# Performance work log

Measured on AMD Instinct MI355X. Metric: run time of the kernel, lower is better.

## Reference

```python
import jax, jax.numpy as jnp
import numpy as np

B, C, H, W = 8, 256, 64, 64
CQK = C // 8  # 32


def setup_inputs() -> dict:
    key = jax.random.key(0)
    ks = jax.random.split(key, 8)
    s = 0.05
    return {
        "x": jax.random.normal(ks[0], (B, C, H, W), dtype=jnp.float32),
        "wq": jax.random.normal(ks[1], (CQK, C), dtype=jnp.float32) * s,
        "bq": jax.random.normal(ks[2], (CQK,), dtype=jnp.float32) * s,
        "wk": jax.random.normal(ks[3], (CQK, C), dtype=jnp.float32) * s,
        "bk": jax.random.normal(ks[4], (CQK,), dtype=jnp.float32) * s,
        "wv": jax.random.normal(ks[5], (C, C), dtype=jnp.float32) * s,
        "bv": jax.random.normal(ks[6], (C,), dtype=jnp.float32) * s,
        "gamma": jax.random.normal(ks[7], (1,), dtype=jnp.float32),
    }


def reference(x, wq, bq, wk, bk, wv, bv, gamma):
    b, c, h, w = x.shape
    xf = x.reshape(b, c, h * w)  # [B, C, N]
    # conv1d kernel-size-1 == per-token linear over channels
    f = jnp.einsum('oc,bcn->bon', wq, xf) + bq[None, :, None]  # [B, C/8, N]
    g = jnp.einsum('oc,bcn->bon', wk, xf) + bk[None, :, None]  # [B, C/8, N]
    hh = jnp.einsum('oc,bcn->bon', wv, xf) + bv[None, :, None]  # [B, C, N]
    # scores[b, i, j] = sum_o f[b, o, i] * g[b, o, j]; NO 1/sqrt(d) scaling
    scores = jnp.einsum('boi,boj->bij', f, g)  # [B, N, N]
    # softmax over dim=1 (the f/query index axis), as in the original
    beta = jax.nn.softmax(scores, axis=1)
    # o[b, c, j] = gamma * sum_i hh[b, c, i] * beta[b, i, j] + xf
    o = gamma[0] * jnp.einsum('bci,bij->bcj', hh, beta) + xf
    return o.reshape(b, c, h, w)
```

## Files before the change

### kernel.cpp

```cpp
#include <hip/hip_runtime.h>
#include <stdint.h>

#define B_ 8
#define C_ 256
#define N_ 4096
#define LOG2E 1.44269504088896f
#define NSHIFT_L2E (-14.0f * 1.44269504088896f)

typedef _Float16 half8 __attribute__((ext_vector_type(8)));
typedef _Float16 half4 __attribute__((ext_vector_type(4)));
typedef __fp16  fp16x2 __attribute__((ext_vector_type(2)));
typedef float floatx4 __attribute__((ext_vector_type(4)));

__global__ __launch_bounds__(256) void k_wprep(const float* __restrict__ wq, const float* __restrict__ bq,
                                               const float* __restrict__ wk, const float* __restrict__ bk,
                                               const float* __restrict__ wv, const float* __restrict__ bv,
                                               _Float16* __restrict__ Whf, float* __restrict__ Bh) {
    int r = blockIdx.x;
    int t = threadIdx.x;
    const float* src;
    float bias;
    if (r < 32)      { src = wq + r * 256;        bias = bq[r]; }
    else if (r < 64) { src = wk + (r - 32) * 256; bias = bk[r - 32]; }
    else             { src = wv + (r - 64) * 256; bias = bv[r - 64]; }
    Whf[(t >> 3) * 2560 + r * 8 + (t & 7)] = (_Float16)src[t];
    if (t == 0) Bh[r] = bias;
}

__global__ __launch_bounds__(256) void k_proj(const float* __restrict__ x,
                                              const _Float16* __restrict__ Whf,
                                              const float* __restrict__ Bh,
                                              _Float16* __restrict__ Kf,
                                              _Float16* __restrict__ Qf,
                                              _Float16* __restrict__ Vf) {
    __shared__ float xtile[64 * 65];
    __shared__ _Float16 As[64 * 264] __attribute__((aligned(16)));
    int id = blockIdx.x;
    int b  = id & 7;
    int i0 = (id >> 3) * 64;
    int t = threadIdx.x;
    int w = t >> 6, lane = t & 63, col = lane & 15, q = lane >> 4;
    const float* xb = x + (size_t)b * C_ * N_ + i0;
    int cr = t >> 4;
    int ip = (t & 15) * 4;
    float4 r0[4], r1[4];
#pragma unroll
    for (int k = 0; k < 4; ++k)
        r0[k] = *(const float4*)&xb[(size_t)(cr + 16 * k) * N_ + ip];
    for (int cc = 0; cc < 4; ++cc) {
        if (cc < 3) {
#pragma unroll
            for (int k = 0; k < 4; ++k)
                r1[k] = *(const float4*)&xb[(size_t)((cc + 1) * 64 + cr + 16 * k) * N_ + ip];
        }
#pragma unroll
        for (int k = 0; k < 4; ++k)
            *(float4*)&xtile[(cr + 16 * k) * 65 + ip] = r0[k];
        __syncthreads();
        int i = t & 63, cb2 = (t >> 6) * 16;
        float v[16];
#pragma unroll
        for (int k = 0; k < 16; ++k) v[k] = xtile[(cb2 + k) * 65 + i];
        half8 h0, h1;
#pragma unroll
        for (int k = 0; k < 8; ++k) { h0[k] = (_Float16)v[k]; h1[k] = (_Float16)v[8 + k]; }
        *(half8*)&As[i * 264 + cc * 64 + cb2] = h0;
        *(half8*)&As[i * 264 + cc * 64 + cb2 + 8] = h1;
        __syncthreads();
#pragma unroll
        for (int k = 0; k < 4; ++k) r0[k] = r1[k];
    }
    floatx4 acc[4][5];
#pragma unroll
    for (int mt = 0; mt < 4; ++mt)
#pragma unroll
        for (int nt = 0; nt < 5; ++nt) acc[mt][nt] = (floatx4){0.f, 0.f, 0.f, 0.f};
#pragma unroll
    for (int kc = 0; kc < 8; ++kc) {
        half8 a[4], bf[5];
#pragma unroll
        for (int nt = 0; nt < 5; ++nt)
            bf[nt] = *(const half8*)&Whf[(kc * 4 + q) * 2560 + (w * 80 + nt * 16 + col) * 8];
#pragma unroll
        for (int mt = 0; mt < 4; ++mt)
            a[mt] = *(const half8*)&As[(mt * 16 + col) * 264 + kc * 32 + q * 8];
#pragma unroll
        for (int mt = 0; mt < 4; ++mt)
#pragma unroll
            for (int nt = 0; nt < 5; ++nt)
                acc[mt][nt] = __builtin_amdgcn_mfma_f32_16x16x32_f16(a[mt], bf[nt], acc[mt][nt], 0, 0, 0);
    }
#pragma unroll
    for (int nt = 0; nt < 5; ++nt) {
        int n = w * 80 + nt * 16 + col;
        float bias = Bh[n];
        if (n < 32) {
#pragma unroll
            for (int mt = 0; mt < 4; ++mt)
#pragma unroll
                for (int r = 0; r < 4; ++r) {
                    int i = i0 + mt * 16 + q * 4 + r;
                    Kf[((((size_t)b * 128 + (i >> 5)) * 4 + (n >> 3)) * 32 + (i & 31)) * 8 + (n & 7)]
                        = (_Float16)((acc[mt][nt][r] + bias) * LOG2E);
                }
        } else if (n < 64) {
            int n2 = n - 32;
#pragma unroll
            for (int mt = 0; mt < 4; ++mt)
#pragma unroll
                for (int r = 0; r < 4; ++r) {
                    int j = i0 + mt * 16 + q * 4 + r;
                    Qf[((((size_t)b * 128 + (j >> 5)) * 4 + (n2 >> 3)) * 32 + (j & 31)) * 8 + (n2 & 7)]
                        = (_Float16)(acc[mt][nt][r] + bias);
                }
        } else {
            int c = n - 64;
#pragma unroll
            for (int mt = 0; mt < 4; ++mt) {
                int ib = (i0 >> 4) + mt;
                half4 v4;
#pragma unroll
                for (int r = 0; r < 4; ++r) v4[r] = (_Float16)(acc[mt][nt][r] + bias);
                *(half4*)&Vf[(((size_t)b * 256 + ib) * 256 + c) * 16 + q * 4] = v4;
            }
        }
    }
}

#define PS_BUF 4096

#define ATTN_STEP(IT, VCUR, VNXT, ROFF, WOFF)                                     \
    {                                                                             \
        if ((IT) < 63) {                                                          \
            _Pragma("unroll")                                                     \
            for (int ct = 0; ct < 2; ++ct) {                                      \
                VNXT[ct * 2 + 0] = *(const half8*)(pV0 + ct * 256);               \
                VNXT[ct * 2 + 1] = *(const half8*)(pV1 + ct * 256);               \
            }                                                                     \
            pV0 += 16384; pV1 += 16384;                                           \
            aKn0 = *(const half8*)(pK);                                           \
            aKn1 = *(const half8*)(pK + 128);                                     \
            pK += 2048;                                                           \
        }                                                                         \
        _Pragma("unroll")                                                         \
        for (int kk = 0; kk < 2; ++kk) {                                          \
            half8 bfr[4];                                                         \
            _Pragma("unroll")                                                     \
            for (int jt = 0; jt < 4; ++jt)                                        \
                bfr[jt] = *(const half8*)&PsF[(ROFF) + jt * 1024 + (kk ? ro1 : ro0)]; \
            _Pragma("unroll")                                                     \
            for (int ct = 0; ct < 2; ++ct)                                        \
                _Pragma("unroll")                                                 \
                for (int jt = 0; jt < 4; ++jt)                                    \
                    acc[ct][jt] = __builtin_amdgcn_mfma_f32_16x16x32_f16(         \
                        VCUR[ct * 2 + kk], bfr[jt], acc[ct][jt], 0, 0, 0);        \
        }                                                                         \
        if ((IT) < 63) {                                                          \
            _Pragma("unroll")                                                     \
            for (int itl = 0; itl < 2; ++itl) {                                   \
                floatx4 s = __builtin_amdgcn_mfma_f32_16x16x32_f16(               \
                    itl ? aKn1 : aKn0, bq, cns, 0, 0, 0);                         \
                float p0 = exp2f(s[0]);                                           \
                float p1 = exp2f(s[1]);                                           \
                float p2 = exp2f(s[2]);                                           \
                float p3 = exp2f(s[3]);                                           \
                lacc += (p0 + p1) + (p2 + p3);                                    \
                union { fp16x2 v; uint32_t u; } plo, phi;                         \
                plo.v = __builtin_amdgcn_cvt_pkrtz(p0, p1);                       \
                phi.v = __builtin_amdgcn_cvt_pkrtz(p2, p3);                       \
                uint2 pw; pw.x = plo.u; pw.y = phi.u;                             \
                *(uint2*)&PsF[(WOFF) + (itl ? wo1 : wo0)] = pw;                   \
            }                                                                     \
        }                                                                         \
        asm volatile("s_waitcnt lgkmcnt(0)\n\ts_barrier" ::: "memory");           \
    }

__global__ __launch_bounds__(512, 4) void k_attn(const _Float16* __restrict__ Kf,
                                                 const _Float16* __restrict__ Qf,
                                                 const _Float16* __restrict__ Vf,
                                                 const float* __restrict__ x,
                                                 const float* __restrict__ gptr,
                                                 float* __restrict__ out) {
    __shared__ _Float16 PsF[2 * PS_BUF] __attribute__((aligned(16)));
    __shared__ float Lp[2][64];
    int id = blockIdx.x;
    int b  = id & 7;
    int j0 = (id >> 3) * 64;
    int t = threadIdx.x;
    int w = t >> 6, lane = t & 63, col = lane & 15, q = lane >> 4;
    int jts = w & 3, ihs = w >> 2;
    int cw  = w * 32;
    const _Float16* Kfb = Kf + (size_t)b * 131072;
    const _Float16* Qfb = Qf + (size_t)b * 131072;
    const _Float16* Vfb = Vf + (size_t)b * 1048576;
    const _Float16* pK  = Kfb + ((ihs * 4 + q) * 32 + col) * 8;
    const _Float16* pV0 = Vfb + ((q >> 1) * 256 + cw + col) * 16 + (q & 1) * 8;
    const _Float16* pV1 = pV0 + 8192;
    const int cswz = col & 7;
    const int ro0 = col * 64 + ((q ^ cswz) << 3);
    const int ro1 = ro0 ^ 32;
    const int wo0 = (jts * 16 + col) * 64 + (((ihs << 2) ^ (q >> 1) ^ cswz) << 3) + (q & 1) * 4;
    const int wo1 = wo0 ^ 16;
    const floatx4 cns = {NSHIFT_L2E, NSHIFT_L2E, NSHIFT_L2E, NSHIFT_L2E};
    floatx4 acc[2][4];
#pragma unroll
    for (int ct = 0; ct < 2; ++ct)
#pragma unroll
        for (int jt = 0; jt < 4; ++jt) acc[ct][jt] = (floatx4){0.f, 0.f, 0.f, 0.f};
    float lacc = 0.f;
    half8 vA[4], vB[4], aKn0, aKn1;
#pragma unroll
    for (int ct = 0; ct < 2; ++ct) {
        vA[ct * 2 + 0] = *(const half8*)(pV0 + ct * 256);
        vA[ct * 2 + 1] = *(const half8*)(pV1 + ct * 256);
    }
    pV0 += 16384; pV1 += 16384;
    aKn0 = *(const half8*)(pK);
    aKn1 = *(const half8*)(pK + 128);
    pK += 2048;
    int jj = j0 + jts * 16;
    half8 bq = *(const half8*)&Qfb[(((jj >> 5) * 4 + q) * 32 + ((jj & 31) + col)) * 8];
#pragma unroll
    for (int itl = 0; itl < 2; ++itl) {
        floatx4 s = __builtin_amdgcn_mfma_f32_16x16x32_f16(itl ? aKn1 : aKn0, bq, cns, 0, 0, 0);
        float p0 = exp2f(s[0]);
        float p1 = exp2f(s[1]);
        float p2 = exp2f(s[2]);
        float p3 = exp2f(s[3]);
        lacc += (p0 + p1) + (p2 + p3);
        union { fp16x2 v; uint32_t u; } plo, phi;
        plo.v = __builtin_amdgcn_cvt_pkrtz(p0, p1);
        phi.v = __builtin_amdgcn_cvt_pkrtz(p2, p3);
        uint2 pw; pw.x = plo.u; pw.y = phi.u;
        *(uint2*)&PsF[itl ? wo1 : wo0] = pw;
    }
    asm volatile("s_waitcnt lgkmcnt(0)\n\ts_barrier" ::: "memory");
    for (int m = 0; m < 32; ++m) {
        int it = m * 2;
        ATTN_STEP(it,     vA, vB, 0,      PS_BUF)
        ATTN_STEP(it + 1, vB, vA, PS_BUF, 0)
    }
    lacc += __shfl_xor(lacc, 16, 64);
    lacc += __shfl_xor(lacc, 32, 64);
    if (lane < 16) Lp[ihs][jts * 16 + lane] = lacc;
    __syncthreads();
    float gamma = gptr[0];
    const float* xb = x + (size_t)b * C_ * N_;
    float* ob = out + (size_t)b * C_ * N_;
#pragma unroll
    for (int jt = 0; jt < 4; ++jt) {
        int jl = jt * 16 + col;
        float li = 1.0f / (Lp[0][jl] + Lp[1][jl]);
        int j = j0 + jl;
#pragma unroll
        for (int ct = 0; ct < 2; ++ct)
#pragma unroll
            for (int r = 0; r < 4; ++r) {
                int c = cw + ct * 16 + q * 4 + r;
                size_t off = (size_t)c * N_ + j;
                ob[off] = gamma * acc[ct][jt][r] * li + xb[off];
            }
    }
}

extern "C" void kernel_launch(void* const* d_in, const int* in_sizes, int n_in,
                              void* d_out, int out_size, void* d_ws, size_t ws_size,
                              hipStream_t stream) {
    const float* x  = (const float*)d_in[0];
    const float* wq = (const float*)d_in[1];
    const float* bq = (const float*)d_in[2];
    const float* wk = (const float*)d_in[3];
    const float* bk = (const float*)d_in[4];
    const float* wv = (const float*)d_in[5];
    const float* bv = (const float*)d_in[6];
    const float* gm = (const float*)d_in[7];
    float* out = (float*)d_out;
    char* ws = (char*)d_ws;
    _Float16* Vf  = (_Float16*)ws;
    _Float16* Kf  = (_Float16*)(ws + 16777216);
    _Float16* Qf  = (_Float16*)(ws + 18874368);
    _Float16* Whf = (_Float16*)(ws + 20971520);
    float*    Bh  = (float*)(ws + 21135360);

    k_wprep<<<dim3(320), 256, 0, stream>>>(wq, bq, wk, bk, wv, bv, Whf, Bh);
    k_proj<<<dim3(512), 256, 0, stream>>>(x, Whf, Bh, Kf, Qf, Vf);
    k_proj<<<dim3(512), 256, 0, stream>>>(x, Whf, Bh, Kf, Qf, Vf);
    k_attn<<<dim3(512), 512, 0, stream>>>(Kf, Qf, Vf, x, gm, out);
}
```

Measured before the change: 229.8 us.

## Fuse weight conversion into projection kernel, drop duplicate launch, stage K/Q in LDS

Removes the separate weight-prep kernel: the projection kernel now reads fp32 weights and biases directly and converts them to fp16 in registers. It also drops the duplicated k_proj launch, which recomputed the same outputs. K and Q results are staged in shared memory (reusing the x-tile buffer) and written out with coalesced 16-byte stores instead of scattered 2-byte stores. The cost is redundant weight reads and conversions in every block, though the weights are small and likely cached.

```diff
diff --git a/kernel.cpp b/kernel.cpp
--- a/kernel.cpp
+++ b/kernel.cpp
@@ -12,29 +12,17 @@
 typedef __fp16  fp16x2 __attribute__((ext_vector_type(2)));
 typedef float floatx4 __attribute__((ext_vector_type(4)));
 
-__global__ __launch_bounds__(256) void k_wprep(const float* __restrict__ wq, const float* __restrict__ bq,
-                                               const float* __restrict__ wk, const float* __restrict__ bk,
-                                               const float* __restrict__ wv, const float* __restrict__ bv,
-                                               _Float16* __restrict__ Whf, float* __restrict__ Bh) {
-    int r = blockIdx.x;
-    int t = threadIdx.x;
-    const float* src;
-    float bias;
-    if (r < 32)      { src = wq + r * 256;        bias = bq[r]; }
-    else if (r < 64) { src = wk + (r - 32) * 256; bias = bk[r - 32]; }
-    else             { src = wv + (r - 64) * 256; bias = bv[r - 64]; }
-    Whf[(t >> 3) * 2560 + r * 8 + (t & 7)] = (_Float16)src[t];
-    if (t == 0) Bh[r] = bias;
-}
-
 __global__ __launch_bounds__(256) void k_proj(const float* __restrict__ x,
-                                              const _Float16* __restrict__ Whf,
-                                              const float* __restrict__ Bh,
+                                              const float* __restrict__ wq, const float* __restrict__ bq,
+                                              const float* __restrict__ wk, const float* __restrict__ bk,
+                                              const float* __restrict__ wv, const float* __restrict__ bv,
                                               _Float16* __restrict__ Kf,
                                               _Float16* __restrict__ Qf,
                                               _Float16* __restrict__ Vf) {
-    __shared__ float xtile[64 * 65];
+    __shared__ __align__(16) unsigned char smem0[64 * 65 * 4];
     __shared__ _Float16 As[64 * 264] __attribute__((aligned(16)));
+    float* xtile = (float*)smem0;
+    _Float16* kq = (_Float16*)smem0;
     int id = blockIdx.x;
     int b  = id & 7;
     int i0 = (id >> 3) * 64;
@@ -70,6 +58,16 @@
 #pragma unroll
         for (int k = 0; k < 4; ++k) r0[k] = r1[k];
     }
+    const float* wrow[5];
+    float bias[5];
+#pragma unroll
+    for (int nt = 0; nt < 5; ++nt) {
+        int n = w * 80 + nt * 16 + col;
+        if (n < 32)      { wrow[nt] = wq + n * 256;        bias[nt] = bq[n]; }
+        else if (n < 64) { wrow[nt] = wk + (n - 32) * 256; bias[nt] = bk[n - 32]; }
+        else             { wrow[nt] = wv + (n - 64) * 256; bias[nt] = bv[n - 64]; }
+        wrow[nt] += q * 8;
+    }
     floatx4 acc[4][5];
 #pragma unroll
     for (int mt = 0; mt < 4; ++mt)
@@ -79,8 +77,12 @@
     for (int kc = 0; kc < 8; ++kc) {
         half8 a[4], bf[5];
 #pragma unroll
-        for (int nt = 0; nt < 5; ++nt)
-            bf[nt] = *(const half8*)&Whf[(kc * 4 + q) * 2560 + (w * 80 + nt * 16 + col) * 8];
+        for (int nt = 0; nt < 5; ++nt) {
+            float4 f0 = *(const float4*)(wrow[nt] + kc * 32);
+            float4 f1 = *(const float4*)(wrow[nt] + kc * 32 + 4);
+#pragma unroll
+            for (int e = 0; e < 4; ++e) { bf[nt][e] = (_Float16)f0[e]; bf[nt][4 + e] = (_Float16)f1[e]; }
+        }
 #pragma unroll
         for (int mt = 0; mt < 4; ++mt)
             a[mt] = *(const half8*)&As[(mt * 16 + col) * 264 + kc * 32 + q * 8];
@@ -93,25 +95,18 @@
 #pragma unroll
     for (int nt = 0; nt < 5; ++nt) {
         int n = w * 80 + nt * 16 + col;
-        float bias = Bh[n];
-        if (n < 32) {
+        if (n < 64) {
+            int nn = n & 31;
+            int halfsel = (n >= 32) ? 1 : 0;
+            float scale = halfsel ? 1.0f : LOG2E;
 #pragma unroll
             for (int mt = 0; mt < 4; ++mt)
 #pragma unroll
                 for (int r = 0; r < 4; ++r) {
-                    int i = i0 + mt * 16 + q * 4 + r;
-                    Kf[((((size_t)b * 128 + (i >> 5)) * 4 + (n >> 3)) * 32 + (i & 31)) * 8 + (n & 7)]
-                        = (_Float16)((acc[mt][nt][r] + bias) * LOG2E);
-                }
-        } else if (n < 64) {
-            int n2 = n - 32;
-#pragma unroll
-            for (int mt = 0; mt < 4; ++mt)
-#pragma unroll
-                for (int r = 0; r < 4; ++r) {
-                    int j = i0 + mt * 16 + q * 4 + r;
-                    Qf[((((size_t)b * 128 + (j >> 5)) * 4 + (n2 >> 3)) * 32 + (j & 31)) * 8 + (n2 & 7)]
-                        = (_Float16)(acc[mt][nt][r] + bias);
+                    int il = mt * 16 + q * 4 + r;
+                    int idx = halfsel * 2048 + ((il >> 5) * 4 + (nn >> 3)) * 256
+                            + (il & 31) * 8 + (nn & 7);
+                    kq[idx] = (_Float16)((acc[mt][nt][r] + bias[nt]) * scale);
                 }
         } else {
             int c = n - 64;
@@ -120,10 +115,18 @@
                 int ib = (i0 >> 4) + mt;
                 half4 v4;
 #pragma unroll
-                for (int r = 0; r < 4; ++r) v4[r] = (_Float16)(acc[mt][nt][r] + bias);
+                for (int r = 0; r < 4; ++r) v4[r] = (_Float16)(acc[mt][nt][r] + bias[nt]);
                 *(half4*)&Vf[(((size_t)b * 256 + ib) * 256 + c) * 16 + q * 4] = v4;
             }
         }
+    }
+    __syncthreads();
+    {
+        int tt = t & 127;
+        _Float16* dst = (t < 128 ? Kf : Qf) + ((size_t)b * 128 + (i0 >> 5)) * 1024;
+        int src = (t < 128 ? 0 : 2048) + tt * 16;
+        *(half8*)&dst[tt * 16]     = *(const half8*)&kq[src];
+        *(half8*)&dst[tt * 16 + 8] = *(const half8*)&kq[src + 8];
     }
 }
 
@@ -279,11 +282,7 @@
     _Float16* Vf  = (_Float16*)ws;
     _Float16* Kf  = (_Float16*)(ws + 16777216);
     _Float16* Qf  = (_Float16*)(ws + 18874368);
-    _Float16* Whf = (_Float16*)(ws + 20971520);
-    float*    Bh  = (float*)(ws + 21135360);
-
-    k_wprep<<<dim3(320), 256, 0, stream>>>(wq, bq, wk, bk, wv, bv, Whf, Bh);
-    k_proj<<<dim3(512), 256, 0, stream>>>(x, Whf, Bh, Kf, Qf, Vf);
-    k_proj<<<dim3(512), 256, 0, stream>>>(x, Whf, Bh, Kf, Qf, Vf);
+
+    k_proj<<<dim3(512), 256, 0, stream>>>(x, wq, bq, wk, bk, wv, bv, Kf, Qf, Vf);
     k_attn<<<dim3(512), 512, 0, stream>>>(Kf, Qf, Vf, x, gm, out);
 }
```

Result: faster. 216.6 us (-5.7%).
